# Kernel optimization log

Measured on AMD Instinct MI355X. Metric: run time of the kernel, lower is better.

The kernel has to match this reference:

```python
import jax, jax.numpy as jnp
import numpy as np

N = 50000
E = 800000
IN_DIM = 128
OUT_DIM = 128


def setup_inputs() -> dict:
    key = jax.random.key(0)
    k1, k2, k3, k4 = jax.random.split(key, 4)
    x = jax.random.normal(k1, (N, IN_DIM), dtype=jnp.float32)
    edge_index = jax.random.randint(k2, (2, E), 0, N, dtype=jnp.int64)
    # Linear(in_dim*2, out_dim) params
    W = jax.random.normal(k3, (2 * IN_DIM, OUT_DIM), dtype=jnp.float32) * (1.0 / np.sqrt(2 * IN_DIM))
    b = jax.random.normal(k4, (OUT_DIM,), dtype=jnp.float32) * 0.01
    return {"x": x, "edge_index": edge_index, "W": W, "b": b}


def reference(x, edge_index, W, b):
    src, dst = edge_index[0], edge_index[1]
    diff = x[src] - x[dst]                              # (E, C)
    # segment-max over destination nodes; empty segments get -inf identity
    seg_max = jax.ops.segment_max(diff, dst, num_segments=N)  # (N, C)
    counts = jax.ops.segment_sum(jnp.ones((E,), dtype=jnp.int32), dst, num_segments=N)
    # original code leaves zeros for nodes with no incoming edges
    max_diff = jnp.where((counts > 0)[:, None], seg_max, jnp.zeros_like(seg_max))
    x_cat = jnp.concatenate([x, max_diff], axis=-1)     # (N, 2C)
    return x_cat @ W + b
```

## Files before the change

kernel.cpp:

```cpp
#include <hip/hip_runtime.h>
#include <math.h>

#define NN 50000
#define NE 800000
#define CD 128
#define PB 3200

typedef __attribute__((ext_vector_type(8))) short short8;
typedef __attribute__((ext_vector_type(4))) float f32x4;
typedef unsigned long long ull;


__device__ inline unsigned pack2bf(float lo, float hi) {
    unsigned a = __float_as_uint(lo), b = __float_as_uint(hi);
    a = (a + 0x7fffu + ((a >> 16) & 1u)) >> 16;
    b = (b + 0x7fffu + ((b >> 16) & 1u)) & 0xffff0000u;
    return a | b;
}

__device__ inline unsigned short f2bf(float f) {
    unsigned u = __float_as_uint(f);
    return (unsigned short)((u + 0x7fffu + ((u >> 16) & 1u)) >> 16);
}

__device__ inline void fmax8(float* m, uint4 v) {
    m[0] = fmaxf(m[0], __uint_as_float(v.x << 16));
    m[1] = fmaxf(m[1], __uint_as_float(v.x & 0xffff0000u));
    m[2] = fmaxf(m[2], __uint_as_float(v.y << 16));
    m[3] = fmaxf(m[3], __uint_as_float(v.y & 0xffff0000u));
    m[4] = fmaxf(m[4], __uint_as_float(v.z << 16));
    m[5] = fmaxf(m[5], __uint_as_float(v.z & 0xffff0000u));
    m[6] = fmaxf(m[6], __uint_as_float(v.w << 16));
    m[7] = fmaxf(m[7], __uint_as_float(v.w & 0xffff0000u));
}


__global__ __launch_bounds__(256) void prep3_k(const int* __restrict__ ei,
                                               const float* __restrict__ x,
                                               const float* __restrict__ W,
                                               int* __restrict__ head,
                                               ull* __restrict__ nxt2,
                                               unsigned* __restrict__ xb,
                                               unsigned short* __restrict__ wt) {
    int tid0 = blockIdx.x * 256 + threadIdx.x;
    int phase = blockIdx.x & 1;

    for (int p = 0; p < 2; p++) {
        if ((p ^ phase) == 0) {
            for (int e = tid0; e < NE; e += PB * 256) {
                int d = ei[NE + e];
                unsigned s = (unsigned)ei[e];
                int old = atomicExch(&head[d], e);
                nxt2[e] = ((ull)s << 32) | (unsigned)old;
            }
        } else {
            for (int i = tid0; i < NN * CD / 4; i += PB * 256) {
                float4 v = ((const float4*)x)[i];
                uint2 r;
                r.x = pack2bf(v.x, v.y);
                r.y = pack2bf(v.z, v.w);
                ((uint2*)xb)[i] = r;
            }
        }
    }
    for (int i = tid0; i < 2 * CD * CD; i += PB * 256) {
        int n = i >> 8, k = i & 255;
        wt[(size_t)n * 256 + k] = f2bf(W[(size_t)k * 128 + n]);
    }
}


__global__ __launch_bounds__(512) void fused_k(const unsigned* __restrict__ xb,
                                               const int* __restrict__ head,
                                               const ull* __restrict__ nxt2,
                                               const short* __restrict__ wt,
                                               const float* __restrict__ bias,
                                               float* __restrict__ out) {
    __shared__ unsigned short idx[64][72];
    __shared__ unsigned short deg[64];
    __shared__ int ovf[64];
    __shared__ unsigned short amx[64][136];

    int t = threadIdx.x;
    int nbase = blockIdx.x * 64;

    if (t < 64) {
        int node = nbase + t;
        int e = (node < NN) ? head[node] : -1;
        int cnt = 0;
        while (e >= 0 && cnt < 64) {
            ull v = nxt2[e];
            idx[t][cnt] = (unsigned short)(v >> 32);
            e = (int)(unsigned)(v & 0xffffffffu);
            cnt++;
        }
        deg[t] = (unsigned short)cnt;
        ovf[t] = e;
    }
    __syncthreads();

    int w = t >> 6, lane = t & 63;
    int q = lane >> 4, c = lane & 15;
#pragma unroll 1
    for (int j = 0; j < 2; j++) {
        int ln = w * 8 + j * 4 + q;
        int node = nbase + ln;
        int cnt = deg[ln];
        float m[8];
#pragma unroll
        for (int i = 0; i < 8; i++) m[i] = -INFINITY;

        for (int base = 0; base < cnt; base += 8) {
            uint4 pk = *(const uint4*)&idx[ln][base];
            int s0 = (int)(pk.x & 0xffffu), s1 = (int)(pk.x >> 16);
            int s2 = (int)(pk.y & 0xffffu), s3 = (int)(pk.y >> 16);
            int s4 = (int)(pk.z & 0xffffu), s5 = (int)(pk.z >> 16);
            int s6 = (int)(pk.w & 0xffffu), s7 = (int)(pk.w >> 16);
            if (base + 8 <= cnt) {
                fmax8(m, *(const uint4*)(xb + (size_t)s0 * 64 + c * 4));
                fmax8(m, *(const uint4*)(xb + (size_t)s1 * 64 + c * 4));
                fmax8(m, *(const uint4*)(xb + (size_t)s2 * 64 + c * 4));
                fmax8(m, *(const uint4*)(xb + (size_t)s3 * 64 + c * 4));
                fmax8(m, *(const uint4*)(xb + (size_t)s4 * 64 + c * 4));
                fmax8(m, *(const uint4*)(xb + (size_t)s5 * 64 + c * 4));
                fmax8(m, *(const uint4*)(xb + (size_t)s6 * 64 + c * 4));
                fmax8(m, *(const uint4*)(xb + (size_t)s7 * 64 + c * 4));
            } else {
                if (base + 0 < cnt) fmax8(m, *(const uint4*)(xb + (size_t)s0 * 64 + c * 4));
                if (base + 1 < cnt) fmax8(m, *(const uint4*)(xb + (size_t)s1 * 64 + c * 4));
                if (base + 2 < cnt) fmax8(m, *(const uint4*)(xb + (size_t)s2 * 64 + c * 4));
                if (base + 3 < cnt) fmax8(m, *(const uint4*)(xb + (size_t)s3 * 64 + c * 4));
                if (base + 4 < cnt) fmax8(m, *(const uint4*)(xb + (size_t)s4 * 64 + c * 4));
                if (base + 5 < cnt) fmax8(m, *(const uint4*)(xb + (size_t)s5 * 64 + c * 4));
                if (base + 6 < cnt) fmax8(m, *(const uint4*)(xb + (size_t)s6 * 64 + c * 4));
                if (base + 7 < cnt) fmax8(m, *(const uint4*)(xb + (size_t)s7 * 64 + c * 4));
            }
        }
        int e = ovf[ln];
        while (e >= 0) {
            ull v = nxt2[e];
            int s = (int)(v >> 32);
            fmax8(m, *(const uint4*)(xb + (size_t)s * 64 + c * 4));
            e = (int)(unsigned)(v & 0xffffffffu);
        }
        uint4 r = make_uint4(0u, 0u, 0u, 0u);
        if (cnt > 0) {
            uint4 xd = *(const uint4*)(xb + (size_t)node * 64 + c * 4);
            float d0 = m[0] - __uint_as_float(xd.x << 16);
            float d1 = m[1] - __uint_as_float(xd.x & 0xffff0000u);
            float d2 = m[2] - __uint_as_float(xd.y << 16);
            float d3 = m[3] - __uint_as_float(xd.y & 0xffff0000u);
            float d4 = m[4] - __uint_as_float(xd.z << 16);
            float d5 = m[5] - __uint_as_float(xd.z & 0xffff0000u);
            float d6 = m[6] - __uint_as_float(xd.w << 16);
            float d7 = m[7] - __uint_as_float(xd.w & 0xffff0000u);
            r.x = pack2bf(d0, d1);
            r.y = pack2bf(d2, d3);
            r.z = pack2bf(d4, d5);
            r.w = pack2bf(d6, d7);
        }
        *(uint4*)&amx[ln][c * 8] = r;
    }
    __syncthreads();

    int mm = lane & 15, g = lane >> 4;
    int rt = w & 3, ch = w >> 2;
    int r0 = nbase + rt * 16;
    int row = r0 + mm;
    bool rowok = row < NN;

    f32x4 acc[4];
#pragma unroll
    for (int ct = 0; ct < 4; ct++) {
        float bv = bias[ch * 64 + ct * 16 + mm];
        acc[ct] = (f32x4){bv, bv, bv, bv};
    }

    const short* xbs = (const short*)xb;
#pragma unroll
    for (int kc = 0; kc < 8; kc++) {
        int k0 = kc * 32;
        short8 a;
        if (kc < 4) {
            a = (short8){0, 0, 0, 0, 0, 0, 0, 0};
            if (rowok) a = *(const short8*)(xbs + (size_t)row * 128 + k0 + g * 8);
        } else {
            a = *(const short8*)&amx[rt * 16 + mm][(k0 - 128) + g * 8];
        }
#pragma unroll
        for (int ct = 0; ct < 4; ct++) {
            short8 b = *(const short8*)(wt + (size_t)(ch * 64 + ct * 16 + mm) * 256 + k0 + g * 8);
            acc[ct] = __builtin_amdgcn_mfma_f32_16x16x32_bf16(a, b, acc[ct], 0, 0, 0);
        }
    }

#pragma unroll
    for (int ct = 0; ct < 4; ct++) {
#pragma unroll
        for (int i = 0; i < 4; i++) {
            int rr = r0 + g * 4 + i;
            if (rr < NN) out[(size_t)rr * 128 + ch * 64 + ct * 16 + mm] = acc[ct][i];
        }
    }
}


extern "C" void kernel_launch(void* const* d_in, const int* in_sizes, int n_in,
                              void* d_out, int out_size, void* d_ws, size_t ws_size,
                              hipStream_t stream) {
    const float* x = (const float*)d_in[0];
    const int* ei = (const int*)d_in[1];
    const float* W = (const float*)d_in[2];
    const float* bias = (const float*)d_in[3];
    float* out = (float*)d_out;

    int* wsi = (int*)d_ws;
    int* head = wsi;
    ull* nxt2 = (ull*)(wsi + 50048);
    unsigned* xb  = (unsigned*)(wsi + 1650048);
    unsigned short* wt = (unsigned short*)(wsi + 4850048);

    hipMemsetAsync(head, 0xFF, NN * sizeof(int), stream);

    prep3_k<<<PB, 256, 0, stream>>>(ei, x, W, head, nxt2, xb, wt);
    fused_k<<<(NN + 63) / 64, 512, 0, stream>>>(xb, head, nxt2, (const short*)wt,
                                                bias, out);
}
```

Baseline: 185.4 us.

## Replace linked-list edge chains with fixed-capacity per-node buckets and overflow list

The per-destination linked list built with atomicExch is replaced by atomicAdd counters that place source indices straight into fixed 64-slot per-node buckets, with a global overflow list for rarely seen high-degree nodes. The fused kernel reads bucket rows directly instead of walking pointer chains serially in a single wavefront, which removes dependent-load latency and the 8-byte next-pointer traffic. Blocks shrink to 32 nodes and 256 threads to raise occupancy. In exchange, overflow handling scans the whole overflow list per node, and the 16-bit packing of destination and source in the overflow entries truncates node ids above 65535, which is fine here because N is 50000.

```diff
diff --git a/kernel.cpp b/kernel.cpp
--- a/kernel.cpp
+++ b/kernel.cpp
@@ -5,6 +5,7 @@
 #define NE 800000
 #define CD 128
 #define PB 3200
+#define OVCAP 65536
 
 typedef __attribute__((ext_vector_type(8))) short short8;
 typedef __attribute__((ext_vector_type(4))) float f32x4;
@@ -35,23 +36,29 @@
 }
 
 
-__global__ __launch_bounds__(256) void prep3_k(const int* __restrict__ ei,
-                                               const float* __restrict__ x,
-                                               const float* __restrict__ W,
-                                               int* __restrict__ head,
-                                               ull* __restrict__ nxt2,
-                                               unsigned* __restrict__ xb,
-                                               unsigned short* __restrict__ wt) {
+__global__ __launch_bounds__(256) void prep_k(const int* __restrict__ ei,
+                                              const float* __restrict__ x,
+                                              const float* __restrict__ W,
+                                              int* __restrict__ cnt,
+                                              unsigned short* __restrict__ bkt,
+                                              unsigned* __restrict__ ovl,
+                                              unsigned* __restrict__ xb,
+                                              unsigned short* __restrict__ wt) {
     int tid0 = blockIdx.x * 256 + threadIdx.x;
     int phase = blockIdx.x & 1;
 
     for (int p = 0; p < 2; p++) {
         if ((p ^ phase) == 0) {
             for (int e = tid0; e < NE; e += PB * 256) {
+                int s = ei[e];
                 int d = ei[NE + e];
-                unsigned s = (unsigned)ei[e];
-                int old = atomicExch(&head[d], e);
-                nxt2[e] = ((ull)s << 32) | (unsigned)old;
+                int k = atomicAdd(&cnt[d], 1);
+                if (k < 64) {
+                    bkt[(size_t)d * 64 + k] = (unsigned short)s;
+                } else {
+                    unsigned oi = atomicAdd((unsigned*)&cnt[NN], 1u);
+                    if (oi < OVCAP) ovl[oi] = ((unsigned)d << 16) | (unsigned)s;
+                }
             }
         } else {
             for (int i = tid0; i < NN * CD / 4; i += PB * 256) {
@@ -70,53 +77,38 @@
 }
 
 
-__global__ __launch_bounds__(512) void fused_k(const unsigned* __restrict__ xb,
-                                               const int* __restrict__ head,
-                                               const ull* __restrict__ nxt2,
+__global__ __launch_bounds__(256) void fused_k(const unsigned* __restrict__ xb,
+                                               const int* __restrict__ cnt,
+                                               const unsigned short* __restrict__ bkt,
+                                               const unsigned* __restrict__ ovl,
                                                const short* __restrict__ wt,
                                                const float* __restrict__ bias,
                                                float* __restrict__ out) {
-    __shared__ unsigned short idx[64][72];
-    __shared__ unsigned short deg[64];
-    __shared__ int ovf[64];
-    __shared__ unsigned short amx[64][136];
+    __shared__ unsigned short amx[32][136];
 
     int t = threadIdx.x;
-    int nbase = blockIdx.x * 64;
-
-    if (t < 64) {
-        int node = nbase + t;
-        int e = (node < NN) ? head[node] : -1;
-        int cnt = 0;
-        while (e >= 0 && cnt < 64) {
-            ull v = nxt2[e];
-            idx[t][cnt] = (unsigned short)(v >> 32);
-            e = (int)(unsigned)(v & 0xffffffffu);
-            cnt++;
-        }
-        deg[t] = (unsigned short)cnt;
-        ovf[t] = e;
-    }
-    __syncthreads();
-
+    int nbase = blockIdx.x * 32;
     int w = t >> 6, lane = t & 63;
     int q = lane >> 4, c = lane & 15;
+
 #pragma unroll 1
     for (int j = 0; j < 2; j++) {
         int ln = w * 8 + j * 4 + q;
         int node = nbase + ln;
-        int cnt = deg[ln];
+        int cntv = (node < NN) ? cnt[node] : 0;
+        int cn = min(cntv, 64);
+        const unsigned short* brow = bkt + (size_t)node * 64;
         float m[8];
 #pragma unroll
         for (int i = 0; i < 8; i++) m[i] = -INFINITY;
 
-        for (int base = 0; base < cnt; base += 8) {
-            uint4 pk = *(const uint4*)&idx[ln][base];
+        for (int base = 0; base < cn; base += 8) {
+            uint4 pk = *(const uint4*)(brow + base);
             int s0 = (int)(pk.x & 0xffffu), s1 = (int)(pk.x >> 16);
             int s2 = (int)(pk.y & 0xffffu), s3 = (int)(pk.y >> 16);
             int s4 = (int)(pk.z & 0xffffu), s5 = (int)(pk.z >> 16);
             int s6 = (int)(pk.w & 0xffffu), s7 = (int)(pk.w >> 16);
-            if (base + 8 <= cnt) {
+            if (base + 8 <= cn) {
                 fmax8(m, *(const uint4*)(xb + (size_t)s0 * 64 + c * 4));
                 fmax8(m, *(const uint4*)(xb + (size_t)s1 * 64 + c * 4));
                 fmax8(m, *(const uint4*)(xb + (size_t)s2 * 64 + c * 4));
@@ -126,25 +118,27 @@
                 fmax8(m, *(const uint4*)(xb + (size_t)s6 * 64 + c * 4));
                 fmax8(m, *(const uint4*)(xb + (size_t)s7 * 64 + c * 4));
             } else {
-                if (base + 0 < cnt) fmax8(m, *(const uint4*)(xb + (size_t)s0 * 64 + c * 4));
-                if (base + 1 < cnt) fmax8(m, *(const uint4*)(xb + (size_t)s1 * 64 + c * 4));
-                if (base + 2 < cnt) fmax8(m, *(const uint4*)(xb + (size_t)s2 * 64 + c * 4));
-                if (base + 3 < cnt) fmax8(m, *(const uint4*)(xb + (size_t)s3 * 64 + c * 4));
-                if (base + 4 < cnt) fmax8(m, *(const uint4*)(xb + (size_t)s4 * 64 + c * 4));
-                if (base + 5 < cnt) fmax8(m, *(const uint4*)(xb + (size_t)s5 * 64 + c * 4));
-                if (base + 6 < cnt) fmax8(m, *(const uint4*)(xb + (size_t)s6 * 64 + c * 4));
-                if (base + 7 < cnt) fmax8(m, *(const uint4*)(xb + (size_t)s7 * 64 + c * 4));
-            }
-        }
-        int e = ovf[ln];
-        while (e >= 0) {
-            ull v = nxt2[e];
-            int s = (int)(v >> 32);
-            fmax8(m, *(const uint4*)(xb + (size_t)s * 64 + c * 4));
-            e = (int)(unsigned)(v & 0xffffffffu);
+                if (base + 0 < cn) fmax8(m, *(const uint4*)(xb + (size_t)s0 * 64 + c * 4));
+                if (base + 1 < cn) fmax8(m, *(const uint4*)(xb + (size_t)s1 * 64 + c * 4));
+                if (base + 2 < cn) fmax8(m, *(const uint4*)(xb + (size_t)s2 * 64 + c * 4));
+                if (base + 3 < cn) fmax8(m, *(const uint4*)(xb + (size_t)s3 * 64 + c * 4));
+                if (base + 4 < cn) fmax8(m, *(const uint4*)(xb + (size_t)s4 * 64 + c * 4));
+                if (base + 5 < cn) fmax8(m, *(const uint4*)(xb + (size_t)s5 * 64 + c * 4));
+                if (base + 6 < cn) fmax8(m, *(const uint4*)(xb + (size_t)s6 * 64 + c * 4));
+                if (base + 7 < cn) fmax8(m, *(const uint4*)(xb + (size_t)s7 * 64 + c * 4));
+            }
+        }
+        if (cntv > 64) {
+            unsigned no = (unsigned)cnt[NN];
+            if (no > OVCAP) no = OVCAP;
+            for (unsigned i2 = 0; i2 < no; i2++) {
+                unsigned u = ovl[i2];
+                if ((int)(u >> 16) == node)
+                    fmax8(m, *(const uint4*)(xb + (size_t)(u & 0xffffu) * 64 + c * 4));
+            }
         }
         uint4 r = make_uint4(0u, 0u, 0u, 0u);
-        if (cnt > 0) {
+        if (cntv > 0) {
             uint4 xd = *(const uint4*)(xb + (size_t)node * 64 + c * 4);
             float d0 = m[0] - __uint_as_float(xd.x << 16);
             float d1 = m[1] - __uint_as_float(xd.x & 0xffff0000u);
@@ -164,7 +158,7 @@
     __syncthreads();
 
     int mm = lane & 15, g = lane >> 4;
-    int rt = w & 3, ch = w >> 2;
+    int rt = w & 1, ch = w >> 1;
     int r0 = nbase + rt * 16;
     int row = r0 + mm;
     bool rowok = row < NN;
@@ -215,14 +209,15 @@
     float* out = (float*)d_out;
 
     int* wsi = (int*)d_ws;
-    int* head = wsi;
-    ull* nxt2 = (ull*)(wsi + 50048);
-    unsigned* xb  = (unsigned*)(wsi + 1650048);
-    unsigned short* wt = (unsigned short*)(wsi + 4850048);
-
-    hipMemsetAsync(head, 0xFF, NN * sizeof(int), stream);
-
-    prep3_k<<<PB, 256, 0, stream>>>(ei, x, W, head, nxt2, xb, wt);
-    fused_k<<<(NN + 63) / 64, 512, 0, stream>>>(xb, head, nxt2, (const short*)wt,
+    int* cnt = wsi;
+    unsigned short* bkt = (unsigned short*)(wsi + 50016);
+    unsigned* xb = (unsigned*)(wsi + 1650016);
+    unsigned short* wt = (unsigned short*)(wsi + 4850016);
+    unsigned* ovl = (unsigned*)(wsi + 4866400);
+
+    hipMemsetAsync(cnt, 0, 50016 * sizeof(int), stream);
+
+    prep_k<<<PB, 256, 0, stream>>>(ei, x, W, cnt, bkt, ovl, xb, wt);
+    fused_k<<<(NN + 31) / 32, 256, 0, stream>>>(xb, cnt, bkt, ovl, (const short*)wt,
                                                 bias, out);
 }
```

Result: slower. 190.8 us (+2.9%).
